# Performance work log

Hardware: AMD Instinct MI355X
Metric: run time of the kernel (lower is better)

Reference implementation:

```python
import jax, jax.numpy as jnp
import numpy as np

NEG_INF = jnp.float32(-2**32 + 1)  # matches the module's padding constant


def setup_inputs() -> dict:
    key = jax.random.key(0)
    ks = jax.random.split(key, 20)
    T, N, E, R = 4, 20000, 320000, 2
    Din, Dh, H = 64, 64, 4
    s = 0.1  # xavier-ish scale
    inp = {
        "x": jax.random.normal(ks[0], (T, N, Din), jnp.float32),
        "edge_index": jax.random.randint(ks[1], (T, R, 2, E), 0, N, jnp.int32),
        "W_src": jax.random.normal(ks[2], (R, Din, H * Dh), jnp.float32) * s,
        "W_dst": jax.random.normal(ks[3], (R, Din, H * Dh), jnp.float32) * s,
        "att_src": jax.random.normal(ks[4], (R, H, Dh), jnp.float32) * s,
        "att_dst": jax.random.normal(ks[5], (R, H, Dh), jnp.float32) * s,
        "ra_W1": jax.random.normal(ks[6], (Dh, 4 * Dh), jnp.float32) * s,
        "ra_b1": jnp.zeros((4 * Dh,), jnp.float32),
        "ra_W2": jax.random.normal(ks[7], (4 * Dh, 1), jnp.float32) * s,
        "lstm_Wih": jax.random.normal(ks[8], (4 * Dh, Dh), jnp.float32) * s,
        "lstm_Whh": jax.random.normal(ks[9], (4 * Dh, Dh), jnp.float32) * s,
        "lstm_bih": jnp.zeros((4 * Dh,), jnp.float32),
        "lstm_bhh": jnp.zeros((4 * Dh,), jnp.float32),
        "pos_emb": jax.random.normal(ks[10], (T, Dh), jnp.float32) * s,
        "Wq": jax.random.normal(ks[11], (Dh, Dh), jnp.float32) * s,
        "Wk": jax.random.normal(ks[12], (Dh, Dh), jnp.float32) * s,
        "Wv": jax.random.normal(ks[13], (Dh, Dh), jnp.float32) * s,
    }
    return inp


def _gat(xt, ei, Ws, Wd, a_s, a_d, N, H, C):
    # PyG GATConv, concat=False, bias=False, eval mode (no dropout)
    src, dst = ei[0], ei[1]
    hs = (xt @ Ws).reshape(N, H, C)
    hd = (xt @ Wd).reshape(N, H, C)
    als = (hs * a_s[None]).sum(-1)          # [N,H]
    ald = (hd * a_d[None]).sum(-1)          # [N,H]
    e = jax.nn.leaky_relu(als[src] + ald[dst], 0.2)   # [E,H]
    m = jax.ops.segment_max(e, dst, num_segments=N)   # [N,H]
    p = jnp.exp(e - m[dst])
    denom = jax.ops.segment_sum(p, dst, num_segments=N)
    alpha = p / (denom[dst] + 1e-16)
    out = jax.ops.segment_sum(hs[src] * alpha[:, :, None], dst, num_segments=N)  # [N,H,C]
    return out.mean(1)                      # concat=False -> mean over heads


def reference(x, edge_index, W_src, W_dst, att_src, att_dst,
              ra_W1, ra_b1, ra_W2,
              lstm_Wih, lstm_Whh, lstm_bih, lstm_bhh,
              pos_emb, Wq, Wk, Wv):
    T, N, _ = x.shape
    R, H, C = att_src.shape   # C == n_hid (per-head GAT channels)

    # ---- intra-relation aggregation: GATConv per etype, vmapped over timeframes
    intra = []
    for r in range(R):
        f = jax.vmap(lambda xt, ei, r=r: _gat(xt, ei, W_src[r], W_dst[r],
                                              att_src[r], att_dst[r], N, H, C))
        intra.append(f(x, edge_index[:, r]))      # [T,N,C]
    h = jnp.stack(intra, axis=2)                  # [T,N,R,C]

    # ---- inter-relation aggregation (RelationAgg), batched over timeframes
    s = jnp.tanh(h @ ra_W1 + ra_b1) @ ra_W2       # [T,N,R,1]
    beta = jax.nn.softmax(s.mean(1), axis=1)      # mean over nodes, softmax over R -> [T,R,1]
    inter = (beta[:, None] * h).sum(2)            # [T,N,C]

    # ---- LSTM over time (batch = nodes)
    def step(carry, xt):
        hh, cc = carry
        g = xt @ lstm_Wih.T + hh @ lstm_Whh.T + lstm_bih + lstm_bhh
        i, f_, gg, o = jnp.split(g, 4, axis=-1)   # torch gate order i,f,g,o
        cc = jax.nn.sigmoid(f_) * cc + jax.nn.sigmoid(i) * jnp.tanh(gg)
        hh = jax.nn.sigmoid(o) * jnp.tanh(cc)
        return (hh, cc), hh
    z = jnp.zeros((N, C), x.dtype)
    _, hs_seq = jax.lax.scan(step, (z, z), inter)  # [T,N,C]
    feats = hs_seq.transpose(1, 0, 2)              # [N,T,C]

    # ---- temporal multi-head attention with causal mask, eval mode
    Ch = C // H
    ti = feats + pos_emb[None]                     # positions are just arange(T)
    qh = (ti @ Wq).reshape(N, T, H, Ch)
    kh = (ti @ Wk).reshape(N, T, H, Ch)
    vh = (ti @ Wv).reshape(N, T, H, Ch)
    scores = jnp.einsum('nqhc,nkhc->nhqk', qh, kh) / jnp.sqrt(jnp.float32(T))
    mask = jnp.tril(jnp.ones((T, T), bool))
    scores = jnp.where(mask[None, None], scores, NEG_INF)
    a = jax.nn.softmax(scores, axis=-1)
    out = jnp.einsum('nhqk,nkhc->nqhc', a, vh).reshape(N, T, C)
    return out  # output_features[ttype][ntype] == out[:, i, :]
```

## Files before the change

kernel.cpp:

```cpp
#include <hip/hip_runtime.h>
#include <hip/hip_bf16.h>

#define T_ 4
#define N_ 20000
#define E_ 320000
#define R_ 2
#define DIN 64
#define G_ 256
#define P_ 8
#define BPAD 18432
#define NB_ 32
#define EPB_ 10000
#define CHN_ 625

typedef unsigned short u16;
typedef __attribute__((ext_vector_type(8))) short bf16x8;
typedef __attribute__((ext_vector_type(2))) _Float16 h2;
typedef __attribute__((ext_vector_type(4))) float f32x4;

__device__ __forceinline__ float bf2f(u16 u) {
    unsigned int i = ((unsigned int)u) << 16; float f;
    __builtin_memcpy(&f, &i, 4); return f;
}
__device__ __forceinline__ u16 f2bf(float f) {
    unsigned int i; __builtin_memcpy(&i, &f, 4);
    unsigned int r = i + 0x7fffu + ((i >> 16) & 1u);
    return (u16)(r >> 16);
}
__device__ __forceinline__ u16 f2h(float f) {
    union { _Float16 h; u16 u; } c; c.h = (_Float16)f; return c.u;
}
__device__ __forceinline__ float sigm(float x) { return 1.f / (1.f + __expf(-x)); }
__device__ __forceinline__ float ftanh(float x) { return 1.f - 2.f / (__expf(2.f * x) + 1.f); }
__device__ __forceinline__ float rdlanef(float v, int l) {
    int i; __builtin_memcpy(&i, &v, 4);
    int r = __builtin_amdgcn_readlane(i, l);
    float f; __builtin_memcpy(&f, &r, 4); return f;
}
__device__ __forceinline__ float fdot2(h2 a, h2 b, float c) {
#if __has_builtin(__builtin_amdgcn_fdot2)
    return __builtin_amdgcn_fdot2(a, b, c, false);
#else
    float r;
    asm("v_dot2_f32_f16 %0, %1, %2, %3" : "=v"(r) : "v"(a), "v"(b), "v"(c));
    return r;
#endif
}
__device__ __forceinline__ unsigned cvtpk_bf16(float lo, float hi) {
    unsigned r;
    asm("v_cvt_pk_bf16_f32 %0, %1, %2" : "=v"(r) : "v"(lo), "v"(hi));
    return r;
}

__device__ __forceinline__ void gemm_direct(
    const u16* __restrict__ A, const u16* __restrict__ Bpad,
    int M, int Astride, int kchunks, int m0, f32x4* acc)
{
    const int tid = threadIdx.x;
    const int lane = tid & 63, wv = tid >> 6;
    const int col = lane & 15, quad = lane >> 4;
    #pragma unroll
    for (int cf = 0; cf < 16; ++cf) { acc[cf][0]=0.f; acc[cf][1]=0.f; acc[cf][2]=0.f; acc[cf][3]=0.f; }

    int row = m0 + wv * 16 + col;
    int row_c = (row < M) ? row : (M - 1);

    for (int kc = 0; kc < kchunks; ++kc) {
        #pragma unroll
        for (int ks = 0; ks < 2; ++ks) {
            bf16x8 a = *(const bf16x8*)(A + (size_t)row_c * Astride + kc * 64 + ks * 32 + quad * 8);
            const u16* bb = Bpad + kc * BPAD + ks * 32 + quad * 8;
            #pragma unroll
            for (int cf = 0; cf < 16; ++cf) {
                bf16x8 b = *(const bf16x8*)(bb + (cf * 16 + col) * 72);
                acc[cf] = __builtin_amdgcn_mfma_f32_16x16x32_bf16(a, b, acc[cf], 0, 0, 0);
            }
        }
    }
}

__global__ __launch_bounds__(256) void k_fold(
    const float* __restrict__ x, const float* __restrict__ wdall,
    float* __restrict__ als_all, float* __restrict__ ald_all, u16* __restrict__ x_h)
{
    __shared__ float wds[1024];
    {
        int tid = threadIdx.x;
        *(float4*)(wds + tid * 4) = *(const float4*)(wdall + tid * 4);
    }
    __syncthreads();

    int t = blockIdx.y;
    int idx = blockIdx.x * 256 + threadIdx.x;
    if (idx >= N_ * 4) return;
    int n = idx >> 2, q = idx & 3;
    const float* xr = x + ((size_t)t * N_ + n) * 64 + q * 16;
    float4 xv[4];
    #pragma unroll
    for (int i = 0; i < 4; ++i) xv[i] = *(const float4*)(xr + i * 4);

    {
        union { u16 h[16]; ushort4 s4[4]; } cv;
        #pragma unroll
        for (int i = 0; i < 4; ++i) {
            cv.h[i*4+0] = f2h(xv[i].x); cv.h[i*4+1] = f2h(xv[i].y);
            cv.h[i*4+2] = f2h(xv[i].z); cv.h[i*4+3] = f2h(xv[i].w);
        }
        u16* xo = x_h + ((size_t)t * N_ + n) * 64 + q * 16;
        #pragma unroll
        for (int i = 0; i < 4; ++i) *(ushort4*)(xo + i * 4) = cv.s4[i];
    }

    float s[16];
    #pragma unroll
    for (int i = 0; i < 16; ++i) s[i] = 0.f;
    #pragma unroll
    for (int i = 0; i < 4; ++i) {
        float xe[4] = {xv[i].x, xv[i].y, xv[i].z, xv[i].w};
        #pragma unroll
        for (int e = 0; e < 4; ++e) {
            int k = q * 16 + i * 4 + e;
            float xk = xe[e];
            #pragma unroll
            for (int tb = 0; tb < 4; ++tb) {
                float4 w = *(const float4*)(wds + tb * 256 + k * 4);
                s[tb*4+0] += xk * w.x; s[tb*4+1] += xk * w.y;
                s[tb*4+2] += xk * w.z; s[tb*4+3] += xk * w.w;
            }
        }
    }
    #pragma unroll
    for (int i = 0; i < 16; ++i) {
        s[i] += __shfl_xor(s[i], 1);
        s[i] += __shfl_xor(s[i], 2);
    }
    if (q == 0) {
        *(float4*)(als_all + ((size_t)(t*2+0) * N_ + n) * 4) = make_float4(s[0], s[1], s[2], s[3]);
        *(float4*)(als_all + ((size_t)(t*2+1) * N_ + n) * 4) = make_float4(s[4], s[5], s[6], s[7]);
        *(float4*)(ald_all + ((size_t)(t*2+0) * N_ + n) * 4) = make_float4(s[8], s[9], s[10], s[11]);
        *(float4*)(ald_all + ((size_t)(t*2+1) * N_ + n) * 4) = make_float4(s[12], s[13], s[14], s[15]);
    }
}

__global__ void k_prep(const float* __restrict__ Wdst, const float* __restrict__ att_dst,
                       const float* __restrict__ Wih, const float* __restrict__ Whh,
                       const float* __restrict__ bih, const float* __restrict__ bhh,
                       const float* __restrict__ Wsrc, const float* __restrict__ att_src,
                       const float* __restrict__ raW1,
                       const float* __restrict__ Wq, const float* __restrict__ Wk,
                       const float* __restrict__ Wv,
                       float* __restrict__ wdall, float* __restrict__ biasv,
                       u16* __restrict__ raW1_pad, u16* __restrict__ Wc_pad,
                       u16* __restrict__ qkv_pad, u16* __restrict__ postB_pad)
{
    int tid = threadIdx.x, bid = blockIdx.x;
    if (bid == 0) {
        int k = tid >> 2, h = tid & 3;
        for (int r = 0; r < 2; ++r) {
            float ss = 0.f, sd = 0.f;
            for (int c = 0; c < 64; ++c) {
                ss += Wsrc[((size_t)r * 64 + k) * 256 + h * 64 + c] * att_src[r * 256 + h * 64 + c];
                sd += Wdst[((size_t)r * 64 + k) * 256 + h * 64 + c] * att_dst[r * 256 + h * 64 + c];
            }
            wdall[r * 256 + k * 4 + h] = ss;
            wdall[512 + r * 256 + k * 4 + h] = sd;
        }
        biasv[tid] = bih[tid] + bhh[tid];
    }
    for (int i = bid * 256 + tid; i < BPAD; i += gridDim.x * 256) {
        int n = i / 72, kk = i % 72;
        raW1_pad[i] = (kk < 64) ? f2bf(raW1[kk * 256 + n]) : (u16)0;
    }
    for (int i = bid * 256 + tid; i < 2 * BPAD; i += gridDim.x * 256) {
        int kc = i / BPAD, q = i % BPAD, n = q / 72, kk = q % 72;
        const float* W = kc ? Whh : Wih;
        Wc_pad[i] = (kk < 64) ? f2bf(W[n * 64 + kk]) : (u16)0;
    }
    for (int i = bid * 256 + tid; i < 192 * 72; i += gridDim.x * 256) {
        int g = i / 72, kk = i % 72;
        int j = g >> 6, c = g & 63;
        const float* W = (j == 0) ? Wq : (j == 1) ? Wk : Wv;
        qkv_pad[i] = (kk < 64) ? f2bf(W[kk * 64 + c]) : (u16)0;
    }
    for (int i = bid * 256 + tid; i < 2 * 4 * 4608; i += gridDim.x * 256) {
        int r = i / 18432, q = i % 18432, kc = q / 4608, qq = q % 4608;
        int c = qq / 72, kk = qq % 72;
        postB_pad[i] = (kk < 64) ? f2bf(Wsrc[(size_t)r * 16384 + kk * 256 + kc * 64 + c]) : (u16)0;
    }
}

__global__ __launch_bounds__(256) void k_hist(const int* __restrict__ ei,
                                              u16* __restrict__ rank, u16* __restrict__ partial)
{
    __shared__ unsigned int hist[N_ / 2];
    int b = blockIdx.x, p = blockIdx.y, tid = threadIdx.x;
    for (int i = tid; i < N_ / 2; i += 256) hist[i] = 0u;
    __syncthreads();
    const int* dsts = ei + ((size_t)p * 2 + 1) * E_ + b * EPB_;
    u16* rk = rank + (size_t)p * E_ + b * EPB_;
    for (int e = tid; e < EPB_; e += 256) {
        int dst = dsts[e];
        unsigned sh = (unsigned)(dst & 1) * 16u;
        unsigned old = atomicAdd(&hist[dst >> 1], 1u << sh);
        rk[e] = (u16)((old >> sh) & 0xffffu);
    }
    __syncthreads();
    u16* part = partial + ((size_t)p * NB_ + b) * N_;
    for (int n = tid; n < N_; n += 256) {
        unsigned hv = hist[n >> 1];
        part[n] = (u16)((hv >> ((unsigned)(n & 1) * 16u)) & 0xffffu);
    }
}

__global__ __launch_bounds__(256) void k_scan1(u16* __restrict__ partial,
                                               int* __restrict__ offsets, int* __restrict__ chunktot)
{
    int p = blockIdx.y, ch = blockIdx.x;
    int tid = threadIdx.x, lane = tid & 63, wid = tid >> 6;
    __shared__ int wtot[4];
    u16* part = partial + (size_t)p * NB_ * N_;
    int* ofs = offsets + (size_t)p * (N_ + 1);
    int n0 = ch * CHN_;
    int carry = 0;
    for (int rnd = 0; rnd < 3; ++rnd) {
        int i = rnd * 256 + tid;
        int n = n0 + i;
        int v = 0;
        if (i < CHN_) {
            int run = 0;
            #pragma unroll 8
            for (int b = 0; b < NB_; ++b) {
                int pv = part[b * N_ + n];
                part[b * N_ + n] = (u16)run;
                run += pv;
            }
            v = run;
        }
        int incl = v;
        for (int d = 1; d < 64; d <<= 1) { int u = __shfl_up(incl, d); if (lane >= d) incl += u; }
        if (lane == 63) wtot[wid] = incl;
        __syncthreads();
        if (tid < 4) {
            int iv = wtot[tid];
            for (int d = 1; d < 4; d <<= 1) { int u = __shfl_up(iv, d); if (tid >= d) iv += u; }
            wtot[tid] = iv;
        }
        __syncthreads();
        int woff = (wid > 0) ? wtot[wid - 1] : 0;
        int tot = wtot[3];
        int excl = carry + woff + incl - v;
        if (i < CHN_) ofs[n] = excl;
        carry += tot;
        __syncthreads();
    }
    if (tid == 0) chunktot[p * NB_ + ch] = carry;
}

__global__ void k_scan3(int* __restrict__ offsets, const int* __restrict__ chunktot) {
    __shared__ int cb[NB_];
    int p = blockIdx.y;
    int tid = threadIdx.x;
    if (tid < 64) {
        int v = (tid < NB_) ? chunktot[p * NB_ + tid] : 0;
        #pragma unroll
        for (int d = 1; d < NB_; d <<= 1) { int u = __shfl_up(v, d); if (tid >= d) v += u; }
        if (tid < NB_) cb[tid] = v;
    }
    __syncthreads();
    int n = blockIdx.x * 256 + tid;
    if (n < N_) {
        int c = n / CHN_;
        int base = (c > 0) ? cb[c - 1] : 0;
        offsets[(size_t)p * (N_ + 1) + n] += base;
    }
    if (n == 0)
        offsets[(size_t)p * (N_ + 1) + N_] = E_;
}

__global__ void k_scatter(const int* __restrict__ ei, const int* __restrict__ offsets,
                          const u16* __restrict__ rank, const u16* __restrict__ partial,
                          u16* __restrict__ csr) {
    int bid = blockIdx.x;
    int p = bid & 7;
    int e = (bid >> 3) * 256 + threadIdx.x;
    int src = ei[((size_t)p * 2 + 0) * E_ + e];
    int dst = ei[((size_t)p * 2 + 1) * E_ + e];
    int b = e / EPB_;
    int pos = offsets[p * (N_ + 1) + dst]
            + (int)partial[((size_t)p * NB_ + b) * N_ + dst]
            + (int)rank[(size_t)p * E_ + e];
    csr[(size_t)p * E_ + pos] = (u16)src;
}

__global__ __launch_bounds__(256) void k_agg(
    const int* __restrict__ offsets, const u16* __restrict__ csr,
    const float* __restrict__ als_all, const float* __restrict__ ald_all,
    const u16* __restrict__ x_h, u16* __restrict__ xagg4)
{
    __shared__ __align__(16) u16 ptab[4][4][64];
    const int bid = blockIdx.x;
    const int p = bid & 7;
    const int t = p >> 1;
    const int* off   = offsets + (size_t)p * (N_ + 1);
    const u16* srcs  = csr + (size_t)p * E_;
    const float* als = als_all + (size_t)p * N_ * 4;
    const float* ald = ald_all + (size_t)p * N_ * 4;
    const u16* xb    = x_h + (size_t)t * N_ * 64;

    const int tid = threadIdx.x, lane = tid & 63, wv = tid >> 6;
    const int g = lane >> 4, el = lane & 15;
    const int n0 = (bid >> 3) * 16 + wv * 4;
    const int ng = n0 + g;
    const int o0 = off[ng], o1 = off[ng + 1];
    const int deg = o1 - o0;
    const float4 aldv = *(const float4*)(ald + (size_t)ng * 4);
    u16* pt = &ptab[wv][0][0];
    const int pw = g * 64 + (el >> 1) * 8 + (el & 1);

    int sdeg[4];
    #pragma unroll
    for (int q = 0; q < 4; ++q) sdeg[q] = __builtin_amdgcn_readlane(deg, q * 16);
    int mdeg = max(max(sdeg[0], sdeg[1]), max(sdeg[2], sdeg[3]));
    int nrounds = (mdeg + 15) >> 4;

    float acc[4][4];
    #pragma unroll
    for (int q = 0; q < 4; ++q)
        #pragma unroll
        for (int h = 0; h < 4; ++h) acc[q][h] = 0.f;
    float d0 = 0.f, d1 = 0.f, d2 = 0.f, d3 = 0.f;

    for (int rr = 0; rr < nrounds; ++rr) {
        int e = rr * 16 + el;
        int sv = 0;
        float p0 = 0.f, p1 = 0.f, p2 = 0.f, p3 = 0.f;
        if (e < deg) {
            sv = (int)srcs[o0 + e];
            float4 av = *(const float4*)(als + (size_t)sv * 4);
            float e0 = av.x + aldv.x, e1 = av.y + aldv.y;
            float e2 = av.z + aldv.z, e3 = av.w + aldv.w;
            e0 = fmaxf(e0, 0.2f * e0); e1 = fmaxf(e1, 0.2f * e1);
            e2 = fmaxf(e2, 0.2f * e2); e3 = fmaxf(e3, 0.2f * e3);
            p0 = __expf(e0); p1 = __expf(e1); p2 = __expf(e2); p3 = __expf(e3);
        }
        d0 += p0; d1 += p1; d2 += p2; d3 += p3;
        pt[pw + 0] = f2h(p0); pt[pw + 2] = f2h(p1);
        pt[pw + 4] = f2h(p2); pt[pw + 6] = f2h(p3);
        #pragma unroll
        for (int q = 0; q < 4; ++q) {
            if (sdeg[q] > rr * 16) {
                const u16* ptq = pt + q * 64;
                #pragma unroll
                for (int pr = 0; pr < 8; ++pr) {
                    int s0i = __builtin_amdgcn_readlane(sv, q * 16 + pr * 2);
                    int s1i = __builtin_amdgcn_readlane(sv, q * 16 + pr * 2 + 1);
                    unsigned x0 = xb[((size_t)(unsigned)s0i << 6) + lane];
                    unsigned x1 = xb[((size_t)(unsigned)s1i << 6) + lane];
                    unsigned xp = x0 | (x1 << 16);
                    uint4 ppv = *(const uint4*)(ptq + pr * 8);
                    h2 xv, q0, q1, q2, q3;
                    __builtin_memcpy(&xv, &xp, 4);
                    __builtin_memcpy(&q0, &ppv.x, 4);
                    __builtin_memcpy(&q1, &ppv.y, 4);
                    __builtin_memcpy(&q2, &ppv.z, 4);
                    __builtin_memcpy(&q3, &ppv.w, 4);
                    acc[q][0] = fdot2(xv, q0, acc[q][0]);
                    acc[q][1] = fdot2(xv, q1, acc[q][1]);
                    acc[q][2] = fdot2(xv, q2, acc[q][2]);
                    acc[q][3] = fdot2(xv, q3, acc[q][3]);
                }
            }
        }
    }
    d0 += __shfl_xor(d0, 1); d0 += __shfl_xor(d0, 2);
    d0 += __shfl_xor(d0, 4); d0 += __shfl_xor(d0, 8);
    d1 += __shfl_xor(d1, 1); d1 += __shfl_xor(d1, 2);
    d1 += __shfl_xor(d1, 4); d1 += __shfl_xor(d1, 8);
    d2 += __shfl_xor(d2, 1); d2 += __shfl_xor(d2, 2);
    d2 += __shfl_xor(d2, 4); d2 += __shfl_xor(d2, 8);
    d3 += __shfl_xor(d3, 1); d3 += __shfl_xor(d3, 2);
    d3 += __shfl_xor(d3, 4); d3 += __shfl_xor(d3, 8);
    #pragma unroll
    for (int q = 0; q < 4; ++q) {
        float s0 = 0.25f / (rdlanef(d0, q * 16) + 1e-16f);
        float s1 = 0.25f / (rdlanef(d1, q * 16) + 1e-16f);
        float s2 = 0.25f / (rdlanef(d2, q * 16) + 1e-16f);
        float s3 = 0.25f / (rdlanef(d3, q * 16) + 1e-16f);
        unsigned w01 = cvtpk_bf16(acc[q][0] * s0, acc[q][1] * s1);
        unsigned w23 = cvtpk_bf16(acc[q][2] * s2, acc[q][3] * s3);
        u16* outp = xagg4 + ((size_t)p * N_ + n0 + q) * 256 + lane;
        outp[0]   = (u16)w01;  outp[64]  = (u16)(w01 >> 16);
        outp[128] = (u16)w23;  outp[192] = (u16)(w23 >> 16);
    }
}

__global__ __launch_bounds__(256) void k_post(
    const u16* __restrict__ xagg4, const u16* __restrict__ postB_pad,
    u16* __restrict__ intra)
{
    const int t = blockIdx.z, r = blockIdx.y;
    const u16* A = xagg4 + ((size_t)(t * 2 + r)) * N_ * 256;
    const u16* Bp = postB_pad + (size_t)r * 4 * 4608;
    const int tid = threadIdx.x, lane = tid & 63, wv = tid >> 6;
    const int col = lane & 15, quad = lane >> 4;
    int m0 = blockIdx.x * 64;
    int row = m0 + wv * 16 + col;
    int row_c = (row < N_) ? row : (N_ - 1);

    f32x4 acc[4];
    #pragma unroll
    for (int cf = 0; cf < 4; ++cf) { acc[cf][0]=0.f; acc[cf][1]=0.f; acc[cf][2]=0.f; acc[cf][3]=0.f; }
    #pragma unroll
    for (int kc = 0; kc < 4; ++kc) {
        #pragma unroll
        for (int ks = 0; ks < 2; ++ks) {
            bf16x8 a = *(const bf16x8*)(A + (size_t)row_c * 256 + kc * 64 + ks * 32 + quad * 8);
            const u16* bb = Bp + kc * 4608 + ks * 32 + quad * 8;
            #pragma unroll
            for (int cf = 0; cf < 4; ++cf) {
                bf16x8 b = *(const bf16x8*)(bb + (cf * 16 + col) * 72);
                acc[cf] = __builtin_amdgcn_mfma_f32_16x16x32_bf16(a, b, acc[cf], 0, 0, 0);
            }
        }
    }
    int rowbase = m0 + wv * 16 + quad * 4;
    #pragma unroll
    for (int cf = 0; cf < 4; ++cf) {
        int c = cf * 16 + col;
        #pragma unroll
        for (int reg = 0; reg < 4; ++reg) {
            int rr = rowbase + reg;
            if (rr < N_)
                intra[(((size_t)t * N_ + rr) * 2 + r) * 64 + c] = f2bf(acc[cf][reg]);
        }
    }
}

__global__ __launch_bounds__(256) void k_relagg(
    const u16* __restrict__ A, const u16* __restrict__ W1pad, const float* __restrict__ b1,
    const float* __restrict__ W2, float* __restrict__ ssum)
{
    int m0 = blockIdx.x * 64;
    f32x4 acc[16];
    gemm_direct(A, W1pad, T_ * N_ * R_, 64, 1, m0, acc);

    const int tid = threadIdx.x, lane = tid & 63, wv = tid >> 6;
    const int col = lane & 15;
    float sp[4] = {0.f, 0.f, 0.f, 0.f};
    #pragma unroll
    for (int cf = 0; cf < 16; ++cf) {
        int gcol = cf * 16 + col;
        float bb = b1[gcol];
        float ww = W2[gcol];
        #pragma unroll
        for (int reg = 0; reg < 4; ++reg)
            sp[reg] += ftanh(acc[cf][reg] + bb) * ww;
    }
    #pragma unroll
    for (int reg = 0; reg < 4; ++reg) {
        float v = sp[reg];
        v += __shfl_xor(v, 1); v += __shfl_xor(v, 2);
        v += __shfl_xor(v, 4); v += __shfl_xor(v, 8);
        sp[reg] = v;
    }
    float se = sp[0] + sp[2];
    float so = sp[1] + sp[3];
    se += __shfl_xor(se, 16); se += __shfl_xor(se, 32);
    so += __shfl_xor(so, 16); so += __shfl_xor(so, 32);
    __shared__ float red[8];
    if (lane == 0) { red[wv * 2] = se; red[wv * 2 + 1] = so; }
    __syncthreads();
    if (tid == 0) {
        float s0 = red[0] + red[2] + red[4] + red[6];
        float s1 = red[1] + red[3] + red[5] + red[7];
        int t = m0 / (N_ * R_);
        atomicAdd(&ssum[t * 2 + 0], s0);
        atomicAdd(&ssum[t * 2 + 1], s1);
    }
}

__global__ __launch_bounds__(256) void k_lstm(
    const u16* __restrict__ intra, const float* __restrict__ ssum,
    const u16* __restrict__ Wc_pad, const float* __restrict__ biasv,
    u16* __restrict__ feats)
{
    __shared__ __align__(16) u16 hl[64][72];
    const int tid = threadIdx.x, lane = tid & 63, wv = tid >> 6;
    const int col = lane & 15, quad = lane >> 4;
    int m0 = blockIdx.x * 64;
    int row = m0 + wv * 16 + col;
    int row_c = (row < N_) ? row : (N_ - 1);
    int rowbase = m0 + wv * 16 + quad * 4;

    float betas[8];
    #pragma unroll
    for (int t = 0; t < 4; ++t) {
        float s0 = ssum[t * 2] * (1.f / N_), s1 = ssum[t * 2 + 1] * (1.f / N_);
        float mx = fmaxf(s0, s1);
        float e0 = __expf(s0 - mx), e1 = __expf(s1 - mx);
        float inv = 1.f / (e0 + e1);
        betas[t * 2] = e0 * inv; betas[t * 2 + 1] = e1 * inv;
    }

    float cc[4][4];
    #pragma unroll
    for (int j = 0; j < 4; ++j)
        #pragma unroll
        for (int reg = 0; reg < 4; ++reg) cc[j][reg] = 0.f;

    for (int t = 0; t < 4; ++t) {
        float b0 = betas[t * 2], b1 = betas[t * 2 + 1];
        const u16* ib = intra + ((size_t)t * N_ + row_c) * 128;

        f32x4 acc[16];
        #pragma unroll
        for (int cf = 0; cf < 16; ++cf) { acc[cf][0]=0.f; acc[cf][1]=0.f; acc[cf][2]=0.f; acc[cf][3]=0.f; }

        #pragma unroll
        for (int ks = 0; ks < 2; ++ks) {
            int coff = ks * 32 + quad * 8;
            bf16x8 i0 = *(const bf16x8*)(ib + coff);
            bf16x8 i1 = *(const bf16x8*)(ib + 64 + coff);
            union { u16 h[8]; bf16x8 v; } cv;
            #pragma unroll
            for (int j = 0; j < 8; ++j)
                cv.h[j] = f2bf(b0 * bf2f((u16)i0[j]) + b1 * bf2f((u16)i1[j]));
            const u16* bb = Wc_pad + ks * 32 + quad * 8;
            #pragma unroll
            for (int cf = 0; cf < 16; ++cf) {
                bf16x8 b = *(const bf16x8*)(bb + (cf * 16 + col) * 72);
                acc[cf] = __builtin_amdgcn_mfma_f32_16x16x32_bf16(cv.v, b, acc[cf], 0, 0, 0);
            }
        }
        if (t > 0) {
            #pragma unroll
            for (int ks = 0; ks < 2; ++ks) {
                bf16x8 a = *(const bf16x8*)&hl[wv * 16 + col][ks * 32 + quad * 8];
                const u16* bb = Wc_pad + BPAD + ks * 32 + quad * 8;
                #pragma unroll
                for (int cf = 0; cf < 16; ++cf) {
                    bf16x8 b = *(const bf16x8*)(bb + (cf * 16 + col) * 72);
                    acc[cf] = __builtin_amdgcn_mfma_f32_16x16x32_bf16(a, b, acc[cf], 0, 0, 0);
                }
            }
        }

        #pragma unroll
        for (int j = 0; j < 4; ++j) {
            int c = j * 16 + col;
            float bi = biasv[c], bf_ = biasv[64 + c], bg = biasv[128 + c], bo = biasv[192 + c];
            #pragma unroll
            for (int reg = 0; reg < 4; ++reg) {
                float gi = acc[j][reg] + bi;
                float gf = acc[j + 4][reg] + bf_;
                float gg = acc[j + 8][reg] + bg;
                float go = acc[j + 12][reg] + bo;
                float c2 = sigm(gf) * cc[j][reg] + sigm(gi) * ftanh(gg);
                float hh = sigm(go) * ftanh(c2);
                cc[j][reg] = c2;
                u16 hb = f2bf(hh);
                hl[wv * 16 + quad * 4 + reg][c] = hb;
                int rr = rowbase + reg;
                if (rr < N_)
                    feats[(size_t)rr * 256 + t * 64 + c] = hb;
            }
        }
    }
}

__global__ __launch_bounds__(256) void k_attn(
    const u16* __restrict__ feats, const float* __restrict__ pos_emb,
    const u16* __restrict__ qkv_pad, float* __restrict__ out)
{
    __shared__ float qkv_s[64 * 200];
    const int tid = threadIdx.x, lane = tid & 63, wv = tid >> 6;
    const int col = lane & 15, quad = lane >> 4;
    int m0 = blockIdx.x * 64;
    int row = m0 + wv * 16 + col;
    int trow = row & 3;

    f32x4 acc[12];
    #pragma unroll
    for (int cf = 0; cf < 12; ++cf) { acc[cf][0]=0.f; acc[cf][1]=0.f; acc[cf][2]=0.f; acc[cf][3]=0.f; }
    #pragma unroll
    for (int ks = 0; ks < 2; ++ks) {
        int coff = ks * 32 + quad * 8;
        bf16x8 fv = *(const bf16x8*)(feats + (size_t)row * 64 + coff);
        float4 p0 = *(const float4*)(pos_emb + trow * 64 + coff);
        float4 p1 = *(const float4*)(pos_emb + trow * 64 + coff + 4);
        union { u16 h[8]; bf16x8 v; } cv;
        cv.h[0] = f2bf(bf2f((u16)fv[0]) + p0.x); cv.h[1] = f2bf(bf2f((u16)fv[1]) + p0.y);
        cv.h[2] = f2bf(bf2f((u16)fv[2]) + p0.z); cv.h[3] = f2bf(bf2f((u16)fv[3]) + p0.w);
        cv.h[4] = f2bf(bf2f((u16)fv[4]) + p1.x); cv.h[5] = f2bf(bf2f((u16)fv[5]) + p1.y);
        cv.h[6] = f2bf(bf2f((u16)fv[6]) + p1.z); cv.h[7] = f2bf(bf2f((u16)fv[7]) + p1.w);
        bf16x8 a = cv.v;
        const u16* bb = qkv_pad + ks * 32 + quad * 8;
        #pragma unroll
        for (int cf = 0; cf < 12; ++cf) {
            bf16x8 b = *(const bf16x8*)(bb + (cf * 16 + col) * 72);
            acc[cf] = __builtin_amdgcn_mfma_f32_16x16x32_bf16(a, b, acc[cf], 0, 0, 0);
        }
    }
    #pragma unroll
    for (int cf = 0; cf < 12; ++cf) {
        int g = cf * 16 + col;
        #pragma unroll
        for (int reg = 0; reg < 4; ++reg) {
            int rl = wv * 16 + quad * 4 + reg;
            qkv_s[rl * 200 + g] = acc[cf][reg];
        }
    }
    __syncthreads();

    int nl = wv * 4 + (lane >> 4);
    int sub = lane & 15;
    int h = sub >> 2, tq = sub & 3;
    const float* qrow = qkv_s + (nl * 4 + tq) * 200 + h * 16;

    float s[4];
    #pragma unroll
    for (int tk = 0; tk < 4; ++tk) {
        const float* krow = qkv_s + (nl * 4 + tk) * 200 + 64 + h * 16;
        float d = 0.f;
        #pragma unroll
        for (int j = 0; j < 16; ++j) d += qrow[j] * krow[j];
        s[tk] = (tk > tq) ? -4294967295.0f : d * 0.5f;
    }
    float mx = fmaxf(fmaxf(s[0], s[1]), fmaxf(s[2], s[3]));
    float a0 = __expf(s[0]-mx), a1 = __expf(s[1]-mx), a2 = __expf(s[2]-mx), a3 = __expf(s[3]-mx);
    float inv = 1.f / (a0 + a1 + a2 + a3);
    a0 *= inv; a1 *= inv; a2 *= inv; a3 *= inv;

    int n = blockIdx.x * 16 + nl;
    const float* v0 = qkv_s + (nl * 4 + 0) * 200 + 128 + h * 16;
    const float* v1 = v0 + 200, *v2 = v0 + 400, *v3 = v0 + 600;
    #pragma unroll
    for (int cc4 = 0; cc4 < 4; ++cc4) {
        float4 o;
        o.x = a0*v0[cc4*4+0] + a1*v1[cc4*4+0] + a2*v2[cc4*4+0] + a3*v3[cc4*4+0];
        o.y = a0*v0[cc4*4+1] + a1*v1[cc4*4+1] + a2*v2[cc4*4+1] + a3*v3[cc4*4+1];
        o.z = a0*v0[cc4*4+2] + a1*v1[cc4*4+2] + a2*v2[cc4*4+2] + a3*v3[cc4*4+2];
        o.w = a0*v0[cc4*4+3] + a1*v1[cc4*4+3] + a2*v2[cc4*4+3] + a3*v3[cc4*4+3];
        *(float4*)(out + (size_t)n * 256 + tq * 64 + h * 16 + cc4 * 4) = o;
    }
}

extern "C" void kernel_launch(void* const* d_in, const int* in_sizes, int n_in,
                              void* d_out, int out_size, void* d_ws, size_t ws_size,
                              hipStream_t stream) {
    const float* x     = (const float*)d_in[0];
    const int* ei      = (const int*)d_in[1];
    const float* Wsrc  = (const float*)d_in[2];
    const float* Wdst  = (const float*)d_in[3];
    const float* att_src = (const float*)d_in[4];
    const float* att_dst = (const float*)d_in[5];
    const float* raW1  = (const float*)d_in[6];
    const float* rab1  = (const float*)d_in[7];
    const float* raW2  = (const float*)d_in[8];
    const float* Wih   = (const float*)d_in[9];
    const float* Whh   = (const float*)d_in[10];
    const float* bih   = (const float*)d_in[11];
    const float* bhh   = (const float*)d_in[12];
    const float* pos   = (const float*)d_in[13];
    const float* Wq    = (const float*)d_in[14];
    const float* Wk    = (const float*)d_in[15];
    const float* Wv    = (const float*)d_in[16];
    float* out = (float*)d_out;

    char* w = (char*)d_ws;
    size_t off = 0;
    auto alloc = [&](size_t bytes) -> char* {
        char* pp = w + off; off += (bytes + 255) & ~(size_t)255; return pp;
    };
    u16*   intra     = (u16*)  alloc((size_t)T_ * N_ * R_ * 64 * 2);
    u16*   x_h       = (u16*)  alloc((size_t)T_ * N_ * 64 * 2);
    float* ssum      = (float*)alloc(256);
    float* wdall     = (float*)alloc(1024 * 4);
    float* biasv     = (float*)alloc(256 * 4);
    u16*   raW1_pad  = (u16*)  alloc(BPAD * 2);
    u16*   Wc_pad    = (u16*)  alloc(2 * BPAD * 2);
    u16*   qkv_pad   = (u16*)  alloc(192 * 72 * 2);
    u16*   postB_pad = (u16*)  alloc(2 * 4 * 4608 * 2);
    int*   chunktot  = (int*)  alloc(P_ * NB_ * 4);
    char*  ubase   = alloc(0);
    size_t uoff = 0;
    auto ualloc = [&](size_t bytes) -> char* {
        char* pp = ubase + uoff; uoff += (bytes + 255) & ~(size_t)255; return pp;
    };
    int*   offsets = (int*)  ualloc((size_t)P_ * (N_ + 1) * 4);
    u16*   csr     = (u16*)  ualloc((size_t)P_ * E_ * 2);
    float* als_all = (float*)ualloc((size_t)P_ * N_ * 4 * 4);
    float* ald_all = (float*)ualloc((size_t)P_ * N_ * 4 * 4);
    u16*   partial = (u16*)  ualloc((size_t)P_ * NB_ * N_ * 2);
    u16*   xagg4   = (u16*)  ualloc((size_t)P_ * N_ * 256 * 2);
    u16*   rank    = (u16*)  xagg4;
    u16*   feats   = (u16*)  ubase;
    (void)ws_size; (void)in_sizes; (void)n_in; (void)out_size;

    k_prep<<<72, 256, 0, stream>>>(Wdst, att_dst, Wih, Whh, bih, bhh, Wsrc, att_src, raW1,
                                   Wq, Wk, Wv, wdall, biasv, raW1_pad, Wc_pad, qkv_pad, postB_pad);
    k_hist<<<dim3(NB_, 8), 256, 0, stream>>>(ei, rank, partial);
    k_scan1<<<dim3(NB_, 8), 256, 0, stream>>>(partial, offsets, chunktot);
    k_scan3<<<dim3(79, 8), 256, 0, stream>>>(offsets, chunktot);
    k_scatter<<<10000, 256, 0, stream>>>(ei, offsets, rank, partial, csr);
    k_fold<<<dim3(313, 4), 256, 0, stream>>>(x, wdall, als_all, ald_all, x_h);
    k_agg<<<10000, 256, 0, stream>>>(offsets, csr, als_all, ald_all, x_h, xagg4);
    k_post<<<dim3(313, 2, 4), 256, 0, stream>>>(xagg4, postB_pad, intra);
    hipMemsetAsync(ssum, 0, 32, stream);
    k_relagg<<<2500, 256, 0, stream>>>(intra, raW1_pad, rab1, raW2, ssum);
    k_lstm<<<313, 256, 0, stream>>>(intra, ssum, Wc_pad, biasv, feats);
    k_attn<<<1250, 256, 0, stream>>>(feats, pos, qkv_pad, out);
}
```

Measured before the change: 450.8 us.

## Batch gather loads in aggregation, vectorize output stores, fold memset into prep

The aggregation inner loop now issues all eight pairs of source-row gathers before the dot products, and skips pairs beyond the remaining degree, so more loads are in flight and padded edges are not fetched. The per-node output is written as one 8-byte store in an interleaved head layout, and the post-GEMM weight padding is permuted to match that layout. The ssum zeroing moves from a separate memset into the prep kernel, removing one launch. The risks are higher register pressure from buffering the loads and the need for the layout change in the two kernels to stay consistent.

```diff
diff --git a/kernel.cpp b/kernel.cpp
--- a/kernel.cpp
+++ b/kernel.cpp
@@ -151,10 +151,12 @@
                        const float* __restrict__ Wv,
                        float* __restrict__ wdall, float* __restrict__ biasv,
                        u16* __restrict__ raW1_pad, u16* __restrict__ Wc_pad,
-                       u16* __restrict__ qkv_pad, u16* __restrict__ postB_pad)
+                       u16* __restrict__ qkv_pad, u16* __restrict__ postB_pad,
+                       float* __restrict__ ssum)
 {
     int tid = threadIdx.x, bid = blockIdx.x;
     if (bid == 0) {
+        if (tid < 8) ssum[tid] = 0.f;
         int k = tid >> 2, h = tid & 3;
         for (int r = 0; r < 2; ++r) {
             float ss = 0.f, sd = 0.f;
@@ -185,7 +187,8 @@
     for (int i = bid * 256 + tid; i < 2 * 4 * 4608; i += gridDim.x * 256) {
         int r = i / 18432, q = i % 18432, kc = q / 4608, qq = q % 4608;
         int c = qq / 72, kk = qq % 72;
-        postB_pad[i] = (kk < 64) ? f2bf(Wsrc[(size_t)r * 16384 + kk * 256 + kc * 64 + c]) : (u16)0;
+        int d = kc * 16 + (kk >> 2), h = kk & 3;
+        postB_pad[i] = (kk < 64) ? f2bf(Wsrc[(size_t)r * 16384 + d * 256 + h * 64 + c]) : (u16)0;
     }
 }
 
@@ -348,26 +351,35 @@
         pt[pw + 4] = f2h(p2); pt[pw + 6] = f2h(p3);
         #pragma unroll
         for (int q = 0; q < 4; ++q) {
-            if (sdeg[q] > rr * 16) {
+            int rem = sdeg[q] - rr * 16;
+            if (rem > 0) {
                 const u16* ptq = pt + q * 64;
+                unsigned xl0[8], xl1[8];
                 #pragma unroll
                 for (int pr = 0; pr < 8; ++pr) {
-                    int s0i = __builtin_amdgcn_readlane(sv, q * 16 + pr * 2);
-                    int s1i = __builtin_amdgcn_readlane(sv, q * 16 + pr * 2 + 1);
-                    unsigned x0 = xb[((size_t)(unsigned)s0i << 6) + lane];
-                    unsigned x1 = xb[((size_t)(unsigned)s1i << 6) + lane];
-                    unsigned xp = x0 | (x1 << 16);
-                    uint4 ppv = *(const uint4*)(ptq + pr * 8);
-                    h2 xv, q0, q1, q2, q3;
-                    __builtin_memcpy(&xv, &xp, 4);
-                    __builtin_memcpy(&q0, &ppv.x, 4);
-                    __builtin_memcpy(&q1, &ppv.y, 4);
-                    __builtin_memcpy(&q2, &ppv.z, 4);
-                    __builtin_memcpy(&q3, &ppv.w, 4);
-                    acc[q][0] = fdot2(xv, q0, acc[q][0]);
-                    acc[q][1] = fdot2(xv, q1, acc[q][1]);
-                    acc[q][2] = fdot2(xv, q2, acc[q][2]);
-                    acc[q][3] = fdot2(xv, q3, acc[q][3]);
+                    if (pr * 2 < rem) {
+                        int s0i = __builtin_amdgcn_readlane(sv, q * 16 + pr * 2);
+                        int s1i = __builtin_amdgcn_readlane(sv, q * 16 + pr * 2 + 1);
+                        xl0[pr] = xb[((size_t)(unsigned)s0i << 6) + lane];
+                        xl1[pr] = xb[((size_t)(unsigned)s1i << 6) + lane];
+                    }
+                }
+                #pragma unroll
+                for (int pr = 0; pr < 8; ++pr) {
+                    if (pr * 2 < rem) {
+                        unsigned xp = xl0[pr] | (xl1[pr] << 16);
+                        uint4 ppv = *(const uint4*)(ptq + pr * 8);
+                        h2 xv, q0, q1, q2, q3;
+                        __builtin_memcpy(&xv, &xp, 4);
+                        __builtin_memcpy(&q0, &ppv.x, 4);
+                        __builtin_memcpy(&q1, &ppv.y, 4);
+                        __builtin_memcpy(&q2, &ppv.z, 4);
+                        __builtin_memcpy(&q3, &ppv.w, 4);
+                        acc[q][0] = fdot2(xv, q0, acc[q][0]);
+                        acc[q][1] = fdot2(xv, q1, acc[q][1]);
+                        acc[q][2] = fdot2(xv, q2, acc[q][2]);
+                        acc[q][3] = fdot2(xv, q3, acc[q][3]);
+                    }
                 }
             }
         }
@@ -380,17 +392,19 @@
     d2 += __shfl_xor(d2, 4); d2 += __shfl_xor(d2, 8);
     d3 += __shfl_xor(d3, 1); d3 += __shfl_xor(d3, 2);
     d3 += __shfl_xor(d3, 4); d3 += __shfl_xor(d3, 8);
+    float inv0 = 0.25f / (d0 + 1e-16f);
+    float inv1 = 0.25f / (d1 + 1e-16f);
+    float inv2 = 0.25f / (d2 + 1e-16f);
+    float inv3 = 0.25f / (d3 + 1e-16f);
     #pragma unroll
     for (int q = 0; q < 4; ++q) {
-        float s0 = 0.25f / (rdlanef(d0, q * 16) + 1e-16f);
-        float s1 = 0.25f / (rdlanef(d1, q * 16) + 1e-16f);
-        float s2 = 0.25f / (rdlanef(d2, q * 16) + 1e-16f);
-        float s3 = 0.25f / (rdlanef(d3, q * 16) + 1e-16f);
+        float s0 = rdlanef(inv0, q * 16);
+        float s1 = rdlanef(inv1, q * 16);
+        float s2 = rdlanef(inv2, q * 16);
+        float s3 = rdlanef(inv3, q * 16);
         unsigned w01 = cvtpk_bf16(acc[q][0] * s0, acc[q][1] * s1);
         unsigned w23 = cvtpk_bf16(acc[q][2] * s2, acc[q][3] * s3);
-        u16* outp = xagg4 + ((size_t)p * N_ + n0 + q) * 256 + lane;
-        outp[0]   = (u16)w01;  outp[64]  = (u16)(w01 >> 16);
-        outp[128] = (u16)w23;  outp[192] = (u16)(w23 >> 16);
+        *(uint2*)(xagg4 + ((size_t)p * N_ + n0 + q) * 256 + lane * 4) = make_uint2(w01, w23);
     }
 }
 
@@ -698,7 +712,8 @@
     (void)ws_size; (void)in_sizes; (void)n_in; (void)out_size;
 
     k_prep<<<72, 256, 0, stream>>>(Wdst, att_dst, Wih, Whh, bih, bhh, Wsrc, att_src, raW1,
-                                   Wq, Wk, Wv, wdall, biasv, raW1_pad, Wc_pad, qkv_pad, postB_pad);
+                                   Wq, Wk, Wv, wdall, biasv, raW1_pad, Wc_pad, qkv_pad,
+                                   postB_pad, ssum);
     k_hist<<<dim3(NB_, 8), 256, 0, stream>>>(ei, rank, partial);
     k_scan1<<<dim3(NB_, 8), 256, 0, stream>>>(partial, offsets, chunktot);
     k_scan3<<<dim3(79, 8), 256, 0, stream>>>(offsets, chunktot);
@@ -706,7 +721,6 @@
     k_fold<<<dim3(313, 4), 256, 0, stream>>>(x, wdall, als_all, ald_all, x_h);
     k_agg<<<10000, 256, 0, stream>>>(offsets, csr, als_all, ald_all, x_h, xagg4);
     k_post<<<dim3(313, 2, 4), 256, 0, stream>>>(xagg4, postB_pad, intra);
-    hipMemsetAsync(ssum, 0, 32, stream);
     k_relagg<<<2500, 256, 0, stream>>>(intra, raW1_pad, rab1, raW2, ssum);
     k_lstm<<<313, 256, 0, stream>>>(intra, ssum, Wc_pad, biasv, feats);
     k_attn<<<1250, 256, 0, stream>>>(feats, pos, qkv_pad, out);
```

After: 438.0 us. 1.03x faster.
